# Kernel tuning notes

Measured on AMD Instinct MI355X. Metric: run time of the kernel, lower is better.

Reference implementation:

```python
import jax, jax.numpy as jnp
import numpy as np

NEMB = 128
N_NODES = 8192
N_EDGES = 16384
N_STEMS = 4096
N_GRAPHS = 256
N_BLOCKS = 105       # BlockDictionary.n_unique_blocks
N_STEMTYPES = 32     # BlockDictionary.n_stem_types
OUT_PER_STEM = 105
OUT_PER_STOP = 1
NUM_CONV_STEPS = 12
SLOPE = 0.01         # nn.LeakyReLU default negative slope


def _act(v):
    return jax.nn.leaky_relu(v, SLOPE)


def setup_inputs() -> dict:
    key = jax.random.key(0)
    ks = jax.random.split(key, 32)
    def p(i, shape, fan_in):
        return jax.random.normal(ks[i], shape, jnp.float32) / np.sqrt(fan_in).astype(np.float32)
    D = NEMB
    inp = {
        "x": jax.random.randint(ks[0], (N_NODES,), 0, N_BLOCKS + 1),
        "stemtypes": jax.random.randint(ks[1], (N_STEMS,), 0, N_STEMTYPES + 1),
        "edge_attr": jax.random.randint(ks[2], (N_EDGES, 2), 0, N_STEMTYPES),
        "edge_index": jax.random.randint(ks[3], (2, N_EDGES), 0, N_NODES),
        "stem_node_idx": jax.random.randint(ks[4], (N_STEMS,), 0, N_NODES),
        "node_batch": jnp.sort(jax.random.randint(ks[5], (N_NODES,), 0, N_GRAPHS)),
        # embedding tables
        "emb_block": p(6, (N_BLOCKS + 1, D), D),
        "emb_stem": p(7, (N_STEMTYPES + 1, D), D),
        "emb_bond": p(8, (N_STEMTYPES, D), D),
        # block2emb MLP
        "b2e_w1": p(9, (D, D), D), "b2e_b1": p(10, (D,), D),
        "b2e_w2": p(11, (D, D), D), "b2e_b2": p(12, (D,), D),
        # NNConv root weight + bias (edge-nn is identity: nn.Sequential())
        "conv_root": p(13, (D, D), D), "conv_bias": p(14, (D,), D),
        # GRU (torch gate order r, z, n)
        "gru_w_ih": p(15, (3 * D, D), D), "gru_w_hh": p(16, (3 * D, D), D),
        "gru_b_ih": p(17, (3 * D,), D), "gru_b_hh": p(18, (3 * D,), D),
        # stem2pred MLP (in = 2*D)
        "s2p_w1": p(19, (D, 2 * D), 2 * D), "s2p_b1": p(20, (D,), 2 * D),
        "s2p_w2": p(21, (D, D), D), "s2p_b2": p(22, (D,), D),
        "s2p_w3": p(23, (OUT_PER_STEM, D), D), "s2p_b3": p(24, (OUT_PER_STEM,), D),
        # global2pred MLP
        "g2p_w1": p(25, (D, D), D), "g2p_b1": p(26, (D,), D),
        "g2p_w2": p(27, (OUT_PER_STOP, D), D), "g2p_b2": p(28, (OUT_PER_STOP,), D),
    }
    return inp


def reference(x, stemtypes, edge_attr, edge_index, stem_node_idx, node_batch,
              emb_block, emb_stem, emb_bond,
              b2e_w1, b2e_b1, b2e_w2, b2e_b2,
              conv_root, conv_bias,
              gru_w_ih, gru_w_hh, gru_b_ih, gru_b_hh,
              s2p_w1, s2p_b1, s2p_w2, s2p_b2, s2p_w3, s2p_b3,
              g2p_w1, g2p_b1, g2p_w2, g2p_b2):
    block_emb = emb_block[x]                          # [N, D]
    stem_emb = emb_stem[stemtypes]                    # [S, D]
    be = emb_bond[edge_attr]                          # [E, 2, D]
    # outer product -> per-edge [D_in, D_out] weight (matches view(-1, in, out))
    W_e = be[:, 0, :, None] * be[:, 1, None, :]       # [E, D, D]

    out = _act(block_emb @ b2e_w1.T + b2e_b1) @ b2e_w2.T + b2e_b2  # [N, D]
    h = out                                           # GRU hidden state

    src, dst = edge_index[0], edge_index[1]
    ones_e = jnp.ones((N_EDGES,), out.dtype)
    deg = jax.ops.segment_sum(ones_e, dst, num_segments=N_NODES)
    inv_deg = jnp.where(deg > 0, 1.0 / jnp.maximum(deg, 1.0), 0.0)[:, None]

    for _ in range(NUM_CONV_STEPS):
        # NNConv: mean_j (x_j @ W_e) + x @ root + bias, then LeakyReLU
        msg = jnp.einsum('ei,eij->ej', out[src], W_e)                  # [E, D]
        agg = jax.ops.segment_sum(msg, dst, num_segments=N_NODES) * inv_deg
        m = _act(agg + out @ conv_root + conv_bias)
        # single-layer GRU, seq_len = 1
        gi = m @ gru_w_ih.T + gru_b_ih
        gh = h @ gru_w_hh.T + gru_b_hh
        ir, iz, inn = jnp.split(gi, 3, axis=-1)
        hr, hz, hn = jnp.split(gh, 3, axis=-1)
        r = jax.nn.sigmoid(ir + hr)
        z = jax.nn.sigmoid(iz + hz)
        n = jnp.tanh(inn + r * hn)
        h = (1.0 - z) * n + z * h
        out = h

    stem_cat = jnp.concatenate([out[stem_node_idx], stem_emb], axis=1)  # [S, 2D]
    s = _act(stem_cat @ s2p_w1.T + s2p_b1)
    s = _act(s @ s2p_w2.T + s2p_b2)
    stem_pred = s @ s2p_w3.T + s2p_b3                                   # [S, out_per_stem]

    # global_mean_pool
    gsum = jax.ops.segment_sum(out, node_batch, num_segments=N_GRAPHS)
    gcnt = jax.ops.segment_sum(jnp.ones((N_NODES,), out.dtype), node_batch, num_segments=N_GRAPHS)
    gmean = gsum / jnp.maximum(gcnt, 1.0)[:, None]
    g = _act(gmean @ g2p_w1.T + g2p_b1)
    stop_pred = g @ g2p_w2.T + g2p_b2                                   # [G, out_per_stop]
    return stem_pred, stop_pred
```

## Files before the change

kernel.cpp:

```cpp
#include <hip/hip_runtime.h>
#include <math.h>

#define D 128
#define NNODES 8192
#define NEDGES 16384
#define NSTEMS 4096
#define NGRAPHS 256
#define NSTEPS 12
#define OPS 105
#define SLOPE 0.01f
#define MT 32
#define NB (NNODES / MT)
#define LDA 136
#define LDA2 264
#define LDQ 40
#define LDH 132

typedef _Float16 half_t;
typedef __attribute__((ext_vector_type(8))) _Float16 f16x8;
typedef __attribute__((ext_vector_type(4))) float f32x4;

__device__ __forceinline__ float leaky(float x) { return x > 0.f ? x : SLOPE * x; }
__device__ __forceinline__ float fast_sigmoid(float x) {
    return __builtin_amdgcn_rcpf(1.f + __expf(-x));
}
__device__ __forceinline__ float fast_tanh(float x) {
    float e = __expf(2.f * x);
    return 1.f - 2.f * __builtin_amdgcn_rcpf(e + 1.f);
}

__global__ void k_setup(
    const float* __restrict__ root, const float* __restrict__ wih,
    const float* __restrict__ whh, const float* __restrict__ bond,
    const float* __restrict__ sw1, const float* __restrict__ sw2,
    const float* __restrict__ sw3, const float* __restrict__ bw1,
    const float* __restrict__ bw2, const float* __restrict__ gw1,
    half_t* __restrict__ rootP, half_t* __restrict__ WihP,
    half_t* __restrict__ WhhP, half_t* __restrict__ bondTP,
    half_t* __restrict__ s1P, half_t* __restrict__ s2P, half_t* __restrict__ s3P,
    half_t* __restrict__ w1P, half_t* __restrict__ w2P, half_t* __restrict__ bondQP,
    float* __restrict__ g1T, int* __restrict__ zeroi) {
    int idx = blockIdx.x * 256 + threadIdx.x;
    int which = blockIdx.y;
    if (which == 10) {
        if (idx < 128 * 128) {
            int r = idx >> 7, c = idx & 127;
            g1T[c * 128 + r] = gw1[idx];
        }
        return;
    }
    if (which == 11) {
        if (idx < 2 * NNODES) zeroi[idx] = 0;
        return;
    }
    int KT = (which == 4) ? 8 : (which == 9) ? 1 : 4;
    int NT = (which == 1 || which == 2) ? 24 : (which == 3) ? 2 : (which == 6) ? 7 : 8;
    if (idx >= NT * KT * 512) return;
    int j = idx & 7;
    int L = (idx >> 3) & 63;
    int t = idx >> 9;
    int kt = t % KT, nt = t / KT;
    int k = kt * 32 + (L >> 4) * 8 + j;
    int n = nt * 16 + (L & 15);
    switch (which) {
        case 0: rootP[idx] = (half_t)root[k * D + n]; break;
        case 1: WihP[idx] = (half_t)wih[n * D + k]; break;
        case 2: WhhP[idx] = (half_t)whh[n * D + k]; break;
        case 3: bondTP[idx] = (half_t)bond[n * D + k]; break;
        case 4: s1P[idx] = (half_t)sw1[n * 256 + k]; break;
        case 5: s2P[idx] = (half_t)sw2[n * 128 + k]; break;
        case 6: s3P[idx] = (n < OPS) ? (half_t)sw3[n * 128 + k] : (half_t)0.f; break;
        case 7: w1P[idx] = (half_t)bw1[n * D + k]; break;
        case 8: w2P[idx] = (half_t)bw2[n * D + k]; break;
        case 9: bondQP[idx] = (half_t)bond[k * D + n]; break;
    }
}

__global__ void k_deg(const int* __restrict__ eidx, int* __restrict__ deg) {
    int e = blockIdx.x * 256 + threadIdx.x;
    if (e < NEDGES) atomicAdd(&deg[eidx[NEDGES + e]], 1);
}

__global__ void k_scan(const int* __restrict__ deg, int* __restrict__ row_start,
                       float* __restrict__ inv_deg) {
    __shared__ int sums[256];
    int t = threadIdx.x;
    int base = t * 32;
    int s = 0;
    for (int k = 0; k < 32; ++k) s += deg[base + k];
    sums[t] = s;
    __syncthreads();
    for (int off = 1; off < 256; off <<= 1) {
        int v = sums[t];
        int u = (t >= off) ? sums[t - off] : 0;
        __syncthreads();
        sums[t] = v + u;
        __syncthreads();
    }
    int run = sums[t] - s;
    for (int k = 0; k < 32; ++k) {
        int d = deg[base + k];
        row_start[base + k] = run;
        run += d;
        inv_deg[base + k] = (d > 0) ? (1.0f / (float)d) : 0.0f;
    }
    if (t == 255) row_start[NNODES] = run;
}

__global__ void k_scatter(const int* __restrict__ eidx, const int* __restrict__ eattr,
                          const int* __restrict__ row_start,
                          int* __restrict__ fill, int4* __restrict__ epack) {
    int e = blockIdx.x * 256 + threadIdx.x;
    if (e < NEDGES) {
        int d = eidx[NEDGES + e];
        int pos = row_start[d] + atomicAdd(&fill[d], 1);
        int2 aa = *(const int2*)(eattr + 2 * e);
        epack[pos] = make_int4(eidx[e], aa.x, aa.y, d);
    }
}

__global__ __launch_bounds__(512, 2) void k_init(
    const int* __restrict__ x, const float* __restrict__ embBlock,
    const half_t* __restrict__ w1P, const float* __restrict__ b1,
    const half_t* __restrict__ w2P, const float* __restrict__ b2,
    const half_t* __restrict__ bondTP,
    float* __restrict__ hF, float* __restrict__ P0) {
    __shared__ __align__(16) half_t Ae[MT * LDA];
    __shared__ __align__(16) half_t T1[MT * LDA];
    const int tid = threadIdx.x;
    const int w = tid >> 6;
    const int lane = tid & 63;
    const int quad = lane >> 4;
    const int l16 = lane & 15;
    const int n0 = blockIdx.x * MT;
    const int c = w * 16 + l16;

    {
        int row = tid >> 4;
        int col = (tid & 15) * 8;
        const float* src = embBlock + (size_t)x[n0 + row] * D + col;
        float4 v0 = ((const float4*)src)[0];
        float4 v1 = ((const float4*)src)[1];
        f16x8 hv;
        hv[0] = (half_t)v0.x; hv[1] = (half_t)v0.y; hv[2] = (half_t)v0.z; hv[3] = (half_t)v0.w;
        hv[4] = (half_t)v1.x; hv[5] = (half_t)v1.y; hv[6] = (half_t)v1.z; hv[7] = (half_t)v1.w;
        *(f16x8*)&Ae[row * LDA + col] = hv;
    }
    __syncthreads();

    {
        f32x4 acc[2] = {{0.f, 0.f, 0.f, 0.f}, {0.f, 0.f, 0.f, 0.f}};
#pragma unroll
        for (int kt = 0; kt < 4; ++kt) {
            f16x8 b = *(const f16x8*)(w1P + (size_t)((w * 4 + kt) * 64 + lane) * 8);
            f16x8 a0 = *(const f16x8*)&Ae[(0 + l16) * LDA + kt * 32 + quad * 8];
            f16x8 a1 = *(const f16x8*)&Ae[(16 + l16) * LDA + kt * 32 + quad * 8];
            acc[0] = __builtin_amdgcn_mfma_f32_16x16x32_f16(a0, b, acc[0], 0, 0, 0);
            acc[1] = __builtin_amdgcn_mfma_f32_16x16x32_f16(a1, b, acc[1], 0, 0, 0);
        }
        float bb = b1[c];
#pragma unroll
        for (int mt = 0; mt < 2; ++mt)
#pragma unroll
            for (int r = 0; r < 4; ++r)
                T1[(mt * 16 + quad * 4 + r) * LDA + c] = (half_t)leaky(acc[mt][r] + bb);
    }
    __syncthreads();

    {
        f32x4 acc[2] = {{0.f, 0.f, 0.f, 0.f}, {0.f, 0.f, 0.f, 0.f}};
#pragma unroll
        for (int kt = 0; kt < 4; ++kt) {
            f16x8 b = *(const f16x8*)(w2P + (size_t)((w * 4 + kt) * 64 + lane) * 8);
            f16x8 a0 = *(const f16x8*)&T1[(0 + l16) * LDA + kt * 32 + quad * 8];
            f16x8 a1 = *(const f16x8*)&T1[(16 + l16) * LDA + kt * 32 + quad * 8];
            acc[0] = __builtin_amdgcn_mfma_f32_16x16x32_f16(a0, b, acc[0], 0, 0, 0);
            acc[1] = __builtin_amdgcn_mfma_f32_16x16x32_f16(a1, b, acc[1], 0, 0, 0);
        }
        float bb = b2[c];
#pragma unroll
        for (int mt = 0; mt < 2; ++mt)
#pragma unroll
            for (int r = 0; r < 4; ++r) {
                int row = mt * 16 + quad * 4 + r;
                float h = acc[mt][r] + bb;
                hF[(size_t)(n0 + row) * D + c] = h;
                Ae[row * LDA + c] = (half_t)h;
            }
    }
    __syncthreads();

    if (w < 4) {
        int mt = w >> 1, nt = w & 1;
        f32x4 acc = {0.f, 0.f, 0.f, 0.f};
#pragma unroll
        for (int kt = 0; kt < 4; ++kt) {
            f16x8 b = *(const f16x8*)(bondTP + (size_t)((nt * 4 + kt) * 64 + lane) * 8);
            f16x8 a = *(const f16x8*)&Ae[(mt * 16 + l16) * LDA + kt * 32 + quad * 8];
            acc = __builtin_amdgcn_mfma_f32_16x16x32_f16(a, b, acc, 0, 0, 0);
        }
#pragma unroll
        for (int r = 0; r < 4; ++r)
            P0[(size_t)(n0 + mt * 16 + quad * 4 + r) * 32 + nt * 16 + l16] = acc[r];
    }
}

__global__ __launch_bounds__(512, 2) void k_step(
    float* __restrict__ hF,
    const float* __restrict__ Pprev, float* __restrict__ Pnext,
    const half_t* __restrict__ rootP, const half_t* __restrict__ WihP,
    const half_t* __restrict__ WhhP, const half_t* __restrict__ bondTP,
    const half_t* __restrict__ bondQP,
    const float* __restrict__ cbias, const float* __restrict__ bih,
    const float* __restrict__ bhh,
    const int4* __restrict__ epack,
    const int* __restrict__ row_start, const float* __restrict__ inv_deg, int writeP) {
    __shared__ __align__(16) half_t As[MT * LDA];
    __shared__ __align__(16) half_t Am[MT * LDA];
    __shared__ __align__(16) float Hs[MT * LDH];
    __shared__ __align__(16) half_t Qh[MT * LDQ];
    __shared__ float Q[MT * 32];

    const int tid = threadIdx.x;
    const int w = tid >> 6;
    const int lane = tid & 63;
    const int quad = lane >> 4;
    const int l16 = lane & 15;
    const int n0 = blockIdx.x * MT;
    const int c = w * 16 + l16;

    {
        int row = tid >> 4;
        int col = (tid & 15) * 8;
        const float* src = hF + (size_t)(n0 + row) * D + col;
        float4 v0 = ((const float4*)src)[0];
        float4 v1 = ((const float4*)src)[1];
        f16x8 hv;
        hv[0] = (half_t)v0.x; hv[1] = (half_t)v0.y; hv[2] = (half_t)v0.z; hv[3] = (half_t)v0.w;
        hv[4] = (half_t)v1.x; hv[5] = (half_t)v1.y; hv[6] = (half_t)v1.z; hv[7] = (half_t)v1.w;
        *(f16x8*)&As[row * LDA + col] = hv;
        *(float4*)&Hs[row * LDH + col] = v0;
        *(float4*)&Hs[row * LDH + col + 4] = v1;
    }
    Q[tid] = 0.f;
    Q[tid + 512] = 0.f;
    const int p0 = row_start[n0];
    const int p1 = row_start[n0 + MT];
    int4 ep;
    float wv = 0.f, idg = 0.f;
    const int pme = p0 + tid;
    const bool have = (pme < p1);
    if (have) {
        ep = epack[pme];
        wv = Pprev[(size_t)ep.x * 32 + ep.y];
        idg = inv_deg[ep.w];
    }
    f16x8 rootB[4], ghB[12], aggB;
#pragma unroll
    for (int kt = 0; kt < 4; ++kt)
        rootB[kt] = *(const f16x8*)(rootP + (size_t)((w * 4 + kt) * 64 + lane) * 8);
#pragma unroll
    for (int kt = 0; kt < 4; ++kt)
#pragma unroll
        for (int g = 0; g < 3; ++g)
            ghB[g * 4 + kt] = *(const f16x8*)(WhhP + (size_t)(((g * 8 + w) * 4 + kt) * 64 + lane) * 8);
    aggB = *(const f16x8*)(bondQP + (size_t)(w * 64 + lane) * 8);
    const float cb = cbias[c];
    const float bi0 = bih[c], bi1 = bih[D + c], bi2 = bih[2 * D + c];
    const float bh0 = bhh[c], bh1 = bhh[D + c], bh2 = bhh[2 * D + c];
    __syncthreads();

    f32x4 convAcc[2] = {{0.f, 0.f, 0.f, 0.f}, {0.f, 0.f, 0.f, 0.f}};
#pragma unroll
    for (int kt = 0; kt < 4; ++kt) {
        f16x8 a0 = *(const f16x8*)&As[(0 + l16) * LDA + kt * 32 + quad * 8];
        f16x8 a1 = *(const f16x8*)&As[(16 + l16) * LDA + kt * 32 + quad * 8];
        convAcc[0] = __builtin_amdgcn_mfma_f32_16x16x32_f16(a0, rootB[kt], convAcc[0], 0, 0, 0);
        convAcc[1] = __builtin_amdgcn_mfma_f32_16x16x32_f16(a1, rootB[kt], convAcc[1], 0, 0, 0);
    }
    if (have) atomicAdd(&Q[(ep.w - n0) * 32 + ep.z], wv * idg);
    for (int p2 = pme + 512; p2 < p1; p2 += 512) {
        int4 e2 = epack[p2];
        atomicAdd(&Q[(e2.w - n0) * 32 + e2.z], Pprev[(size_t)e2.x * 32 + e2.y] * inv_deg[e2.w]);
    }
    f32x4 ghA[2][3];
#pragma unroll
    for (int mt = 0; mt < 2; ++mt)
#pragma unroll
        for (int g = 0; g < 3; ++g) ghA[mt][g] = f32x4{0.f, 0.f, 0.f, 0.f};
#pragma unroll
    for (int kt = 0; kt < 4; ++kt) {
        f16x8 a0 = *(const f16x8*)&As[(0 + l16) * LDA + kt * 32 + quad * 8];
        f16x8 a1 = *(const f16x8*)&As[(16 + l16) * LDA + kt * 32 + quad * 8];
#pragma unroll
        for (int g = 0; g < 3; ++g) {
            ghA[0][g] = __builtin_amdgcn_mfma_f32_16x16x32_f16(a0, ghB[g * 4 + kt], ghA[0][g], 0, 0, 0);
            ghA[1][g] = __builtin_amdgcn_mfma_f32_16x16x32_f16(a1, ghB[g * 4 + kt], ghA[1][g], 0, 0, 0);
        }
    }
    __syncthreads();

    f16x8 giB[12];
#pragma unroll
    for (int kt = 0; kt < 4; ++kt)
#pragma unroll
        for (int g = 0; g < 3; ++g)
            giB[g * 4 + kt] = *(const f16x8*)(WihP + (size_t)(((g * 8 + w) * 4 + kt) * 64 + lane) * 8);

    Qh[(tid >> 5) * LDQ + (tid & 31)] = (half_t)Q[tid];
    Qh[((tid + 512) >> 5) * LDQ + (tid & 31)] = (half_t)Q[tid + 512];
    __syncthreads();

#pragma unroll
    for (int mt = 0; mt < 2; ++mt) {
        f32x4 acc = {0.f, 0.f, 0.f, 0.f};
        f16x8 a = *(const f16x8*)&Qh[(mt * 16 + l16) * LDQ + quad * 8];
        acc = __builtin_amdgcn_mfma_f32_16x16x32_f16(a, aggB, acc, 0, 0, 0);
#pragma unroll
        for (int r = 0; r < 4; ++r) {
            float m = convAcc[mt][r] + cb + acc[r];
            Am[(mt * 16 + quad * 4 + r) * LDA + c] = (half_t)leaky(m);
        }
    }
    __syncthreads();

    f32x4 giA[2][3];
#pragma unroll
    for (int mt = 0; mt < 2; ++mt)
#pragma unroll
        for (int g = 0; g < 3; ++g) giA[mt][g] = f32x4{0.f, 0.f, 0.f, 0.f};
#pragma unroll
    for (int kt = 0; kt < 4; ++kt) {
        f16x8 a0 = *(const f16x8*)&Am[(0 + l16) * LDA + kt * 32 + quad * 8];
        f16x8 a1 = *(const f16x8*)&Am[(16 + l16) * LDA + kt * 32 + quad * 8];
#pragma unroll
        for (int g = 0; g < 3; ++g) {
            giA[0][g] = __builtin_amdgcn_mfma_f32_16x16x32_f16(a0, giB[g * 4 + kt], giA[0][g], 0, 0, 0);
            giA[1][g] = __builtin_amdgcn_mfma_f32_16x16x32_f16(a1, giB[g * 4 + kt], giA[1][g], 0, 0, 0);
        }
    }
#pragma unroll
    for (int mt = 0; mt < 2; ++mt) {
#pragma unroll
        for (int r = 0; r < 4; ++r) {
            int row = mt * 16 + quad * 4 + r;
            float rg = fast_sigmoid(giA[mt][0][r] + bi0 + ghA[mt][0][r] + bh0);
            float z = fast_sigmoid(giA[mt][1][r] + bi1 + ghA[mt][1][r] + bh1);
            float nn = fast_tanh(giA[mt][2][r] + bi2 + rg * (ghA[mt][2][r] + bh2));
            float hnew = (1.f - z) * nn + z * Hs[row * LDH + c];
            hF[(size_t)(n0 + row) * D + c] = hnew;
            As[row * LDA + c] = (half_t)hnew;
        }
    }

    if (writeP) {
        __syncthreads();
        if (w < 4) {
            int mt = w >> 1, nt = w & 1;
            f32x4 acc = {0.f, 0.f, 0.f, 0.f};
#pragma unroll
            for (int kt = 0; kt < 4; ++kt) {
                f16x8 b = *(const f16x8*)(bondTP + (size_t)((nt * 4 + kt) * 64 + lane) * 8);
                f16x8 a = *(const f16x8*)&As[(mt * 16 + l16) * LDA + kt * 32 + quad * 8];
                acc = __builtin_amdgcn_mfma_f32_16x16x32_f16(a, b, acc, 0, 0, 0);
            }
#pragma unroll
            for (int r = 0; r < 4; ++r)
                Pnext[(size_t)(n0 + mt * 16 + quad * 4 + r) * 32 + nt * 16 + l16] = acc[r];
        }
    }
}

__device__ __forceinline__ int lower_bound_dev(const int* a, int n, int v) {
    int lo = 0, hi = n;
    while (lo < hi) {
        int m = (lo + hi) >> 1;
        if (a[m] < v) lo = m + 1;
        else hi = m;
    }
    return lo;
}

__global__ __launch_bounds__(512) void k_heads(
    const float* __restrict__ hF, const int* __restrict__ sni, const int* __restrict__ stypes,
    const float* __restrict__ embStem,
    const half_t* __restrict__ s1P, const float* __restrict__ b1,
    const half_t* __restrict__ s2P, const float* __restrict__ b2,
    const half_t* __restrict__ s3P, const float* __restrict__ b3,
    const int* __restrict__ batch,
    const float* __restrict__ g1T, const float* __restrict__ gb1,
    const float* __restrict__ gw2, const float* __restrict__ gb2,
    float* __restrict__ dout) {
    __shared__ __align__(16) half_t cat[16 * LDA2];
    __shared__ __align__(16) half_t t1[16 * LDA];
    __shared__ __align__(16) half_t t2[16 * LDA];
    const int tid = threadIdx.x;
    if (blockIdx.x >= 256) {
        int g = blockIdx.x - 256;
        if (tid >= 128) return;
        __shared__ float mean_s[D];
        __shared__ float red[D];
        int j = tid;
        int lo = lower_bound_dev(batch, NNODES, g);
        int hi = lower_bound_dev(batch, NNODES, g + 1);
        float sum = 0.f;
        for (int n = lo; n < hi; ++n) sum += hF[(size_t)n * D + j];
        float denom = (hi > lo) ? (float)(hi - lo) : 1.0f;
        mean_s[j] = sum / denom;
        __syncthreads();
        float a = gb1[j];
        for (int i = 0; i < D; ++i) a += mean_s[i] * g1T[i * D + j];
        a = leaky(a);
        red[j] = a * gw2[j];
        __syncthreads();
        for (int off = 64; off > 0; off >>= 1) {
            if (j < off) red[j] += red[j + off];
            __syncthreads();
        }
        if (j == 0) dout[NSTEMS * OPS + g] = red[0] + gb2[0];
        return;
    }
    const int w = tid >> 6;
    const int lane = tid & 63;
    const int quad = lane >> 4;
    const int l16 = lane & 15;
    const int s0 = blockIdx.x * 16;
    const int c = w * 16 + l16;

    {
        int row = tid >> 5;
        int col = (tid & 31) * 8;
        const float* src;
        if (col < D) src = hF + (size_t)sni[s0 + row] * D + col;
        else src = embStem + (size_t)stypes[s0 + row] * D + (col - D);
        float4 v0 = ((const float4*)src)[0];
        float4 v1 = ((const float4*)src)[1];
        f16x8 hv;
        hv[0] = (half_t)v0.x; hv[1] = (half_t)v0.y; hv[2] = (half_t)v0.z; hv[3] = (half_t)v0.w;
        hv[4] = (half_t)v1.x; hv[5] = (half_t)v1.y; hv[6] = (half_t)v1.z; hv[7] = (half_t)v1.w;
        *(f16x8*)&cat[row * LDA2 + col] = hv;
    }
    __syncthreads();

    {
        f32x4 acc = {0.f, 0.f, 0.f, 0.f};
#pragma unroll
        for (int kt = 0; kt < 8; ++kt) {
            f16x8 b = *(const f16x8*)(s1P + (size_t)((w * 8 + kt) * 64 + lane) * 8);
            f16x8 a = *(const f16x8*)&cat[l16 * LDA2 + kt * 32 + quad * 8];
            acc = __builtin_amdgcn_mfma_f32_16x16x32_f16(a, b, acc, 0, 0, 0);
        }
        float bb = b1[c];
#pragma unroll
        for (int r = 0; r < 4; ++r)
            t1[(quad * 4 + r) * LDA + c] = (half_t)leaky(acc[r] + bb);
    }
    __syncthreads();
    {
        f32x4 acc = {0.f, 0.f, 0.f, 0.f};
#pragma unroll
        for (int kt = 0; kt < 4; ++kt) {
            f16x8 b = *(const f16x8*)(s2P + (size_t)((w * 4 + kt) * 64 + lane) * 8);
            f16x8 a = *(const f16x8*)&t1[l16 * LDA + kt * 32 + quad * 8];
            acc = __builtin_amdgcn_mfma_f32_16x16x32_f16(a, b, acc, 0, 0, 0);
        }
        float bb = b2[c];
#pragma unroll
        for (int r = 0; r < 4; ++r)
            t2[(quad * 4 + r) * LDA + c] = (half_t)leaky(acc[r] + bb);
    }
    __syncthreads();
    if (w < 7) {
        f32x4 acc = {0.f, 0.f, 0.f, 0.f};
#pragma unroll
        for (int kt = 0; kt < 4; ++kt) {
            f16x8 b = *(const f16x8*)(s3P + (size_t)((w * 4 + kt) * 64 + lane) * 8);
            f16x8 a = *(const f16x8*)&t2[l16 * LDA + kt * 32 + quad * 8];
            acc = __builtin_amdgcn_mfma_f32_16x16x32_f16(a, b, acc, 0, 0, 0);
        }
        int j = w * 16 + l16;
        if (j < OPS) {
            float bb = b3[j];
#pragma unroll
            for (int r = 0; r < 4; ++r)
                dout[(size_t)(s0 + quad * 4 + r) * OPS + j] = acc[r] + bb;
        }
    }
}

extern "C" void kernel_launch(void* const* d_in, const int* in_sizes, int n_in,
                              void* d_out, int out_size, void* d_ws, size_t ws_size,
                              hipStream_t stream) {
    const int* x = (const int*)d_in[0];
    const int* stypes = (const int*)d_in[1];
    const int* eattr = (const int*)d_in[2];
    const int* eidx = (const int*)d_in[3];
    const int* sni = (const int*)d_in[4];
    const int* batch = (const int*)d_in[5];
    const float* embBlock = (const float*)d_in[6];
    const float* embStem = (const float*)d_in[7];
    const float* embBond = (const float*)d_in[8];
    const float* b2e_w1 = (const float*)d_in[9];
    const float* b2e_b1 = (const float*)d_in[10];
    const float* b2e_w2 = (const float*)d_in[11];
    const float* b2e_b2 = (const float*)d_in[12];
    const float* conv_root = (const float*)d_in[13];
    const float* conv_bias = (const float*)d_in[14];
    const float* gru_w_ih = (const float*)d_in[15];
    const float* gru_w_hh = (const float*)d_in[16];
    const float* gru_b_ih = (const float*)d_in[17];
    const float* gru_b_hh = (const float*)d_in[18];
    const float* s2p_w1 = (const float*)d_in[19];
    const float* s2p_b1 = (const float*)d_in[20];
    const float* s2p_w2 = (const float*)d_in[21];
    const float* s2p_b2 = (const float*)d_in[22];
    const float* s2p_w3 = (const float*)d_in[23];
    const float* s2p_b3 = (const float*)d_in[24];
    const float* g2p_w1 = (const float*)d_in[25];
    const float* g2p_b1 = (const float*)d_in[26];
    const float* g2p_w2 = (const float*)d_in[27];
    const float* g2p_b2 = (const float*)d_in[28];
    float* out_f = (float*)d_out;

    float* W = (float*)d_ws;
    size_t off = 0;
    auto alloc = [&](size_t words) {
        size_t o = off;
        off += (words + 3) & ~(size_t)3;
        return o;
    };
    float* hF = W + alloc(NNODES * D);
    float* P0 = W + alloc(NNODES * 32);
    float* P1 = W + alloc(NNODES * 32);
    half_t* rootP = (half_t*)(W + alloc(16384 / 2));
    half_t* WihP = (half_t*)(W + alloc(49152 / 2));
    half_t* WhhP = (half_t*)(W + alloc(49152 / 2));
    half_t* bondTP = (half_t*)(W + alloc(4096 / 2));
    half_t* s1P = (half_t*)(W + alloc(32768 / 2));
    half_t* s2P = (half_t*)(W + alloc(16384 / 2));
    half_t* s3P = (half_t*)(W + alloc(14336 / 2));
    half_t* w1P = (half_t*)(W + alloc(16384 / 2));
    half_t* w2P = (half_t*)(W + alloc(16384 / 2));
    half_t* bondQP = (half_t*)(W + alloc(4096 / 2));
    float* g1T = W + alloc(128 * 128);
    int* row_start = (int*)(W + alloc(NNODES + 1));
    int4* epack = (int4*)(W + alloc(NEDGES * 4));
    float* inv_deg = W + alloc(NNODES);
    float* zbase = W + alloc(2 * NNODES);
    int* deg = (int*)zbase;
    int* fill = deg + NNODES;

    k_setup<<<dim3(192, 12), 256, 0, stream>>>(
        conv_root, gru_w_ih, gru_w_hh, embBond, s2p_w1, s2p_w2, s2p_w3,
        b2e_w1, b2e_w2, g2p_w1,
        rootP, WihP, WhhP, bondTP, s1P, s2P, s3P, w1P, w2P, bondQP,
        g1T, (int*)zbase);
    k_deg<<<(NEDGES + 255) / 256, 256, 0, stream>>>(eidx, deg);
    k_scan<<<1, 256, 0, stream>>>(deg, row_start, inv_deg);
    k_scatter<<<(NEDGES + 255) / 256, 256, 0, stream>>>(eidx, eattr, row_start, fill, epack);
    k_init<<<NNODES / MT, 512, 0, stream>>>(x, embBlock, w1P, b2e_b1, w2P, b2e_b2,
                                            bondTP, hF, P0);

    for (int step = 0; step < NSTEPS; ++step) {
        const float* Pprev = (step & 1) ? P1 : P0;
        float* Pnext = (step & 1) ? P0 : P1;
        int writeP = (step < NSTEPS - 1) ? 1 : 0;
        k_step<<<NB, 512, 0, stream>>>(
            hF, Pprev, Pnext, rootP, WihP, WhhP, bondTP, bondQP,
            conv_bias, gru_b_ih, gru_b_hh,
            epack, row_start, inv_deg, writeP);
    }

    k_heads<<<NSTEMS / 16 + NGRAPHS, 512, 0, stream>>>(
        hF, sni, stypes, embStem,
        s1P, s2p_b1, s2P, s2p_b2, s3P, s2p_b3,
        batch, g1T, g2p_b1, g2p_w2, g2p_b2, out_f);
}
```

Baseline: 254.1 us.

## Halve k_step node tile to 16 rows and raise occupancy to 4 blocks/CU

The per-step GRU/conv kernel now handles 16 nodes per block instead of 32, which doubles the grid to 512 blocks and raises launch bounds to 4 blocks per CU. GRU weight fragments are streamed from global inside the MFMA loops instead of being preloaded into registers, and the bond-projection B fragments are hoisted to the start. The aim is better CU occupancy and latency hiding for a small grid, at the cost of reloading the weights twice as often per node and each block doing less reuse. With 512 threads per block, edges beyond 512 per tile still fall into the strided loop.

```diff
diff --git a/kernel.cpp b/kernel.cpp
--- a/kernel.cpp
+++ b/kernel.cpp
@@ -11,6 +11,8 @@
 #define SLOPE 0.01f
 #define MT 32
 #define NB (NNODES / MT)
+#define MTS 16
+#define NBS (NNODES / MTS)
 #define LDA 136
 #define LDA2 264
 #define LDQ 40
@@ -18,6 +20,7 @@
 
 typedef _Float16 half_t;
 typedef __attribute__((ext_vector_type(8))) _Float16 f16x8;
+typedef __attribute__((ext_vector_type(4))) _Float16 f16x4;
 typedef __attribute__((ext_vector_type(4))) float f32x4;
 
 __device__ __forceinline__ float leaky(float x) { return x > 0.f ? x : SLOPE * x; }
@@ -205,7 +208,7 @@
     }
 }
 
-__global__ __launch_bounds__(512, 2) void k_step(
+__global__ __launch_bounds__(512, 4) void k_step(
     float* __restrict__ hF,
     const float* __restrict__ Pprev, float* __restrict__ Pnext,
     const half_t* __restrict__ rootP, const half_t* __restrict__ WihP,
@@ -215,158 +218,132 @@
     const float* __restrict__ bhh,
     const int4* __restrict__ epack,
     const int* __restrict__ row_start, const float* __restrict__ inv_deg, int writeP) {
-    __shared__ __align__(16) half_t As[MT * LDA];
-    __shared__ __align__(16) half_t Am[MT * LDA];
-    __shared__ __align__(16) float Hs[MT * LDH];
-    __shared__ __align__(16) half_t Qh[MT * LDQ];
-    __shared__ float Q[MT * 32];
+    __shared__ __align__(16) half_t As[MTS * LDA];
+    __shared__ __align__(16) half_t Am[MTS * LDA];
+    __shared__ __align__(16) float Hs[MTS * LDH];
+    __shared__ __align__(16) half_t Qh[MTS * LDQ];
+    __shared__ float Q[MTS * 32];
 
     const int tid = threadIdx.x;
     const int w = tid >> 6;
     const int lane = tid & 63;
     const int quad = lane >> 4;
     const int l16 = lane & 15;
-    const int n0 = blockIdx.x * MT;
+    const int n0 = blockIdx.x * MTS;
     const int c = w * 16 + l16;
 
     {
-        int row = tid >> 4;
-        int col = (tid & 15) * 8;
+        int row = tid >> 5;
+        int col = (tid & 31) * 4;
         const float* src = hF + (size_t)(n0 + row) * D + col;
-        float4 v0 = ((const float4*)src)[0];
-        float4 v1 = ((const float4*)src)[1];
-        f16x8 hv;
+        float4 v0 = *(const float4*)src;
+        f16x4 hv;
         hv[0] = (half_t)v0.x; hv[1] = (half_t)v0.y; hv[2] = (half_t)v0.z; hv[3] = (half_t)v0.w;
-        hv[4] = (half_t)v1.x; hv[5] = (half_t)v1.y; hv[6] = (half_t)v1.z; hv[7] = (half_t)v1.w;
-        *(f16x8*)&As[row * LDA + col] = hv;
+        *(f16x4*)&As[row * LDA + col] = hv;
         *(float4*)&Hs[row * LDH + col] = v0;
-        *(float4*)&Hs[row * LDH + col + 4] = v1;
     }
     Q[tid] = 0.f;
-    Q[tid + 512] = 0.f;
     const int p0 = row_start[n0];
-    const int p1 = row_start[n0 + MT];
+    const int p1 = row_start[n0 + MTS];
     int4 ep;
-    float wv = 0.f, idg = 0.f;
+    float wv = 0.f;
     const int pme = p0 + tid;
     const bool have = (pme < p1);
     if (have) {
         ep = epack[pme];
-        wv = Pprev[(size_t)ep.x * 32 + ep.y];
-        idg = inv_deg[ep.w];
-    }
-    f16x8 rootB[4], ghB[12], aggB;
+        wv = Pprev[(size_t)ep.x * 32 + ep.y] * inv_deg[ep.w];
+    }
+    f16x8 rootB[4], aggB, bondTB[4];
 #pragma unroll
     for (int kt = 0; kt < 4; ++kt)
         rootB[kt] = *(const f16x8*)(rootP + (size_t)((w * 4 + kt) * 64 + lane) * 8);
-#pragma unroll
-    for (int kt = 0; kt < 4; ++kt)
-#pragma unroll
-        for (int g = 0; g < 3; ++g)
-            ghB[g * 4 + kt] = *(const f16x8*)(WhhP + (size_t)(((g * 8 + w) * 4 + kt) * 64 + lane) * 8);
     aggB = *(const f16x8*)(bondQP + (size_t)(w * 64 + lane) * 8);
+    {
+        const int ntb = w & 1;
+#pragma unroll
+        for (int kt = 0; kt < 4; ++kt)
+            bondTB[kt] = *(const f16x8*)(bondTP + (size_t)((ntb * 4 + kt) * 64 + lane) * 8);
+    }
     const float cb = cbias[c];
     const float bi0 = bih[c], bi1 = bih[D + c], bi2 = bih[2 * D + c];
     const float bh0 = bhh[c], bh1 = bhh[D + c], bh2 = bhh[2 * D + c];
     __syncthreads();
 
-    f32x4 convAcc[2] = {{0.f, 0.f, 0.f, 0.f}, {0.f, 0.f, 0.f, 0.f}};
+    f32x4 convAcc = {0.f, 0.f, 0.f, 0.f};
 #pragma unroll
     for (int kt = 0; kt < 4; ++kt) {
-        f16x8 a0 = *(const f16x8*)&As[(0 + l16) * LDA + kt * 32 + quad * 8];
-        f16x8 a1 = *(const f16x8*)&As[(16 + l16) * LDA + kt * 32 + quad * 8];
-        convAcc[0] = __builtin_amdgcn_mfma_f32_16x16x32_f16(a0, rootB[kt], convAcc[0], 0, 0, 0);
-        convAcc[1] = __builtin_amdgcn_mfma_f32_16x16x32_f16(a1, rootB[kt], convAcc[1], 0, 0, 0);
-    }
-    if (have) atomicAdd(&Q[(ep.w - n0) * 32 + ep.z], wv * idg);
+        f16x8 a = *(const f16x8*)&As[l16 * LDA + kt * 32 + quad * 8];
+        convAcc = __builtin_amdgcn_mfma_f32_16x16x32_f16(a, rootB[kt], convAcc, 0, 0, 0);
+    }
+    if (have) atomicAdd(&Q[(ep.w - n0) * 32 + ep.z], wv);
     for (int p2 = pme + 512; p2 < p1; p2 += 512) {
         int4 e2 = epack[p2];
         atomicAdd(&Q[(e2.w - n0) * 32 + e2.z], Pprev[(size_t)e2.x * 32 + e2.y] * inv_deg[e2.w]);
     }
-    f32x4 ghA[2][3];
-#pragma unroll
-    for (int mt = 0; mt < 2; ++mt)
-#pragma unroll
-        for (int g = 0; g < 3; ++g) ghA[mt][g] = f32x4{0.f, 0.f, 0.f, 0.f};
+    f32x4 ghA[3];
+#pragma unroll
+    for (int g = 0; g < 3; ++g) ghA[g] = f32x4{0.f, 0.f, 0.f, 0.f};
 #pragma unroll
     for (int kt = 0; kt < 4; ++kt) {
-        f16x8 a0 = *(const f16x8*)&As[(0 + l16) * LDA + kt * 32 + quad * 8];
-        f16x8 a1 = *(const f16x8*)&As[(16 + l16) * LDA + kt * 32 + quad * 8];
+        f16x8 a = *(const f16x8*)&As[l16 * LDA + kt * 32 + quad * 8];
 #pragma unroll
         for (int g = 0; g < 3; ++g) {
-            ghA[0][g] = __builtin_amdgcn_mfma_f32_16x16x32_f16(a0, ghB[g * 4 + kt], ghA[0][g], 0, 0, 0);
-            ghA[1][g] = __builtin_amdgcn_mfma_f32_16x16x32_f16(a1, ghB[g * 4 + kt], ghA[1][g], 0, 0, 0);
-        }
-    }
-    __syncthreads();
-
-    f16x8 giB[12];
-#pragma unroll
-    for (int kt = 0; kt < 4; ++kt)
-#pragma unroll
-        for (int g = 0; g < 3; ++g)
-            giB[g * 4 + kt] = *(const f16x8*)(WihP + (size_t)(((g * 8 + w) * 4 + kt) * 64 + lane) * 8);
+            f16x8 b = *(const f16x8*)(WhhP + (size_t)(((g * 8 + w) * 4 + kt) * 64 + lane) * 8);
+            ghA[g] = __builtin_amdgcn_mfma_f32_16x16x32_f16(a, b, ghA[g], 0, 0, 0);
+        }
+    }
+    __syncthreads();
 
     Qh[(tid >> 5) * LDQ + (tid & 31)] = (half_t)Q[tid];
-    Qh[((tid + 512) >> 5) * LDQ + (tid & 31)] = (half_t)Q[tid + 512];
-    __syncthreads();
-
-#pragma unroll
-    for (int mt = 0; mt < 2; ++mt) {
+    __syncthreads();
+
+    {
         f32x4 acc = {0.f, 0.f, 0.f, 0.f};
-        f16x8 a = *(const f16x8*)&Qh[(mt * 16 + l16) * LDQ + quad * 8];
+        f16x8 a = *(const f16x8*)&Qh[l16 * LDQ + quad * 8];
         acc = __builtin_amdgcn_mfma_f32_16x16x32_f16(a, aggB, acc, 0, 0, 0);
 #pragma unroll
         for (int r = 0; r < 4; ++r) {
-            float m = convAcc[mt][r] + cb + acc[r];
-            Am[(mt * 16 + quad * 4 + r) * LDA + c] = (half_t)leaky(m);
-        }
-    }
-    __syncthreads();
-
-    f32x4 giA[2][3];
-#pragma unroll
-    for (int mt = 0; mt < 2; ++mt)
-#pragma unroll
-        for (int g = 0; g < 3; ++g) giA[mt][g] = f32x4{0.f, 0.f, 0.f, 0.f};
+            float m = convAcc[r] + cb + acc[r];
+            Am[(quad * 4 + r) * LDA + c] = (half_t)leaky(m);
+        }
+    }
+    __syncthreads();
+
+    f32x4 giA[3];
+#pragma unroll
+    for (int g = 0; g < 3; ++g) giA[g] = f32x4{0.f, 0.f, 0.f, 0.f};
 #pragma unroll
     for (int kt = 0; kt < 4; ++kt) {
-        f16x8 a0 = *(const f16x8*)&Am[(0 + l16) * LDA + kt * 32 + quad * 8];
-        f16x8 a1 = *(const f16x8*)&Am[(16 + l16) * LDA + kt * 32 + quad * 8];
+        f16x8 a = *(const f16x8*)&Am[l16 * LDA + kt * 32 + quad * 8];
 #pragma unroll
         for (int g = 0; g < 3; ++g) {
-            giA[0][g] = __builtin_amdgcn_mfma_f32_16x16x32_f16(a0, giB[g * 4 + kt], giA[0][g], 0, 0, 0);
-            giA[1][g] = __builtin_amdgcn_mfma_f32_16x16x32_f16(a1, giB[g * 4 + kt], giA[1][g], 0, 0, 0);
-        }
-    }
-#pragma unroll
-    for (int mt = 0; mt < 2; ++mt) {
-#pragma unroll
-        for (int r = 0; r < 4; ++r) {
-            int row = mt * 16 + quad * 4 + r;
-            float rg = fast_sigmoid(giA[mt][0][r] + bi0 + ghA[mt][0][r] + bh0);
-            float z = fast_sigmoid(giA[mt][1][r] + bi1 + ghA[mt][1][r] + bh1);
-            float nn = fast_tanh(giA[mt][2][r] + bi2 + rg * (ghA[mt][2][r] + bh2));
-            float hnew = (1.f - z) * nn + z * Hs[row * LDH + c];
-            hF[(size_t)(n0 + row) * D + c] = hnew;
-            As[row * LDA + c] = (half_t)hnew;
-        }
+            f16x8 b = *(const f16x8*)(WihP + (size_t)(((g * 8 + w) * 4 + kt) * 64 + lane) * 8);
+            giA[g] = __builtin_amdgcn_mfma_f32_16x16x32_f16(a, b, giA[g], 0, 0, 0);
+        }
+    }
+#pragma unroll
+    for (int r = 0; r < 4; ++r) {
+        int row = quad * 4 + r;
+        float rg = fast_sigmoid(giA[0][r] + bi0 + ghA[0][r] + bh0);
+        float z = fast_sigmoid(giA[1][r] + bi1 + ghA[1][r] + bh1);
+        float nn = fast_tanh(giA[2][r] + bi2 + rg * (ghA[2][r] + bh2));
+        float hnew = (1.f - z) * nn + z * Hs[row * LDH + c];
+        hF[(size_t)(n0 + row) * D + c] = hnew;
+        As[row * LDA + c] = (half_t)hnew;
     }
 
     if (writeP) {
         __syncthreads();
-        if (w < 4) {
-            int mt = w >> 1, nt = w & 1;
+        if (w < 2) {
             f32x4 acc = {0.f, 0.f, 0.f, 0.f};
 #pragma unroll
             for (int kt = 0; kt < 4; ++kt) {
-                f16x8 b = *(const f16x8*)(bondTP + (size_t)((nt * 4 + kt) * 64 + lane) * 8);
-                f16x8 a = *(const f16x8*)&As[(mt * 16 + l16) * LDA + kt * 32 + quad * 8];
-                acc = __builtin_amdgcn_mfma_f32_16x16x32_f16(a, b, acc, 0, 0, 0);
+                f16x8 a = *(const f16x8*)&As[l16 * LDA + kt * 32 + quad * 8];
+                acc = __builtin_amdgcn_mfma_f32_16x16x32_f16(a, bondTB[kt], acc, 0, 0, 0);
             }
 #pragma unroll
             for (int r = 0; r < 4; ++r)
-                Pnext[(size_t)(n0 + mt * 16 + quad * 4 + r) * 32 + nt * 16 + l16] = acc[r];
+                Pnext[(size_t)(n0 + quad * 4 + r) * 32 + w * 16 + l16] = acc[r];
         }
     }
 }
@@ -558,14 +535,14 @@
     k_deg<<<(NEDGES + 255) / 256, 256, 0, stream>>>(eidx, deg);
     k_scan<<<1, 256, 0, stream>>>(deg, row_start, inv_deg);
     k_scatter<<<(NEDGES + 255) / 256, 256, 0, stream>>>(eidx, eattr, row_start, fill, epack);
-    k_init<<<NNODES / MT, 512, 0, stream>>>(x, embBlock, w1P, b2e_b1, w2P, b2e_b2,
-                                            bondTP, hF, P0);
+    k_init<<<NB, 512, 0, stream>>>(x, embBlock, w1P, b2e_b1, w2P, b2e_b2,
+                                   bondTP, hF, P0);
 
     for (int step = 0; step < NSTEPS; ++step) {
         const float* Pprev = (step & 1) ? P1 : P0;
         float* Pnext = (step & 1) ? P0 : P1;
         int writeP = (step < NSTEPS - 1) ? 1 : 0;
-        k_step<<<NB, 512, 0, stream>>>(
+        k_step<<<NBS, 512, 0, stream>>>(
             hF, Pprev, Pnext, rootP, WihP, WhhP, bondTP, bondQP,
             conv_bias, gru_b_ih, gru_b_hh,
             epack, row_start, inv_deg, writeP);
```

Measured after the change: 269.6 us. 6.1% more time.
